# Performance work log

Measured on AMD Instinct MI355X. Metric: run time of the kernel, lower is better.

The kernel has to match this reference:

```python
import jax, jax.numpy as jnp
import numpy as np

EULER = 0.5772156649015329  # Euler-Mascheroni constant


def _expi_neg(t):
    """Ei(t) for t < 0, via Ei(t) = -E1(-t).

    E1 uses the power series for x < 8 and the asymptotic expansion for x >= 8.
    This replaces the scipy.special.expi CPU round-trip of the original module.
    """
    x = -t  # x > 0
    # --- series branch (x < 8): E1(x) = -gamma - ln(x) + sum_{k>=1} (-1)^{k+1} x^k/(k*k!)
    xs = jnp.minimum(x, 8.0)
    s = jnp.zeros_like(xs)
    term = xs  # (-1)^{k+1} xs^k / k!  starting at k=1
    for k in range(1, 31):
        s = s + term / k
        term = term * (-xs) / (k + 1)
    e1_small = -EULER - jnp.log(xs) + s
    # --- asymptotic branch (x >= 8): E1(x) ~ e^{-x}/x * sum_n (-1)^n n! / x^n
    xl = jnp.maximum(x, 8.0)
    a = jnp.ones_like(xl)
    acc = jnp.ones_like(xl)
    for n in range(1, 9):
        a = a * (-n) / xl
        acc = acc + a
    e1_large = jnp.exp(-xl) / xl * acc
    e1 = jnp.where(x < 8.0, e1_small, e1_large)
    return -e1


def _li(v):
    # logarithmic integral li(v) = Ei(ln v); constant w.r.t. params (scipy detaches in torch)
    return jax.lax.stop_gradient(_expi_neg(jnp.log(v)))


def _phi(u, var2, var3, var4, var5):
    log_term = jnp.log(1.0 - u)
    li_term = _li(1.0 - u)
    return (var2 / log_term
            + var3 * li_term
            + var4 * ((1.0 - u) / log_term - li_term)
            + var5 * ((1.0 - u) * (log_term + 1.0) / (2.0 * log_term ** 2) - li_term / 2.0))


def setup_inputs() -> dict:
    key = jax.random.key(0)
    B, L, D = 262144, 64, 32
    hidden = [128, 128, 64]
    ks = jax.random.split(key, 16)
    u = jax.random.uniform(ks[0], (B, L), dtype=jnp.float32, minval=1e-4, maxval=1.0 - 1e-4)
    dims = [L] + hidden + [D]
    inp = {"u": u}
    for i in range(4):
        inp[f"W{i}"] = jax.random.normal(ks[1 + 2 * i], (dims[i], dims[i + 1]), dtype=jnp.float32) / np.sqrt(dims[i]).astype(np.float32)
        inp[f"b{i}"] = jnp.zeros((dims[i + 1],), dtype=jnp.float32)
    for j in range(1, 7):
        inp[f"var{j}"] = jax.random.normal(ks[8 + j], (1, D), dtype=jnp.float32) * 0.1
    return inp


def reference(u, W0, b0, W1, b1, W2, b2, W3, b3, var1, var2, var3, var4, var5, var6):
    # MLP: three Linear+ReLU blocks then final Linear to dim_data
    h = u
    for W, b in ((W0, b0), (W1, b1), (W2, b2)):
        h = jax.nn.relu(h @ W + b)
    net = h @ W3 + b3  # (B, dim_data)
    D = net.shape[1]
    ud = u[:, :D]
    # spline corrections
    p01 = -4.0 * ud ** 5 + 5.0 * ud ** 4
    corr1 = jnp.nan_to_num(p01 * (var1 + _phi(ud, var2, var3, var4, var5)), nan=0.0)
    corr2 = var6 * (ud ** 3 - 2.0 * ud ** 2 + ud)
    net_tif = jax.nn.relu(net + corr1 + corr2)
    # inverse TIF activation: ((1 - u^2)/2)^{-x}
    return jnp.power((1.0 - ud ** 2) / 2.0, -net_tif)
```

## Files before the change

kernel.cpp:

```cpp
#include <hip/hip_runtime.h>
#include <hip/hip_bf16.h>
#include <math.h>

#define LN2_F 0.69314718055994531f
#define INV_LN2_F 1.44269504088896341f
#define REGION_HALFS 2048

typedef _Float16 half8 __attribute__((ext_vector_type(8)));
typedef _Float16 h4_t __attribute__((ext_vector_type(4)));
typedef __fp16 pk2_t __attribute__((ext_vector_type(2)));
typedef __attribute__((ext_vector_type(4))) float f32x4;
typedef __attribute__((ext_vector_type(8))) short short8;

#define MFMA16(a, b, c) __builtin_amdgcn_mfma_f32_16x16x32_f16((a), (b), (c), 0, 0, 0)

__global__ void prep_weights(const float* __restrict__ W0, const float* __restrict__ W1,
                             const float* __restrict__ W2, const float* __restrict__ W3,
                             short* __restrict__ ws) {
    int e = blockIdx.x * 256 + threadIdx.x;
    const float* W; int N, NT, base, ul;
    if (e < 1024)      { W = W0; N = 128; NT = 8; base = 0;     ul = e; }
    else if (e < 3072) { W = W1; N = 128; NT = 8; base = 8192;  ul = e - 1024; }
    else if (e < 4096) { W = W2; N = 64;  NT = 4; base = 24576; ul = e - 3072; }
    else if (e < 4352) { W = W3; N = 32;  NT = 2; base = 32768; ul = e - 4096; }
    else return;
    const int cp = ul >> 6, lane = ul & 63;
    const int s = cp / NT, ct = cp % NT;
    const int k0 = s * 32 + (lane >> 4) * 8;
    const int n = ct * 16 + (lane & 15);
    union { half8 h; short8 s; } v;
#pragma unroll
    for (int j = 0; j < 8; ++j) v.h[j] = (_Float16)W[(size_t)(k0 + j) * N + n];
    *(short8*)(ws + base + cp * 512 + lane * 8) = v.s;
}


__device__ __forceinline__ void lds_fence() {
    asm volatile("s_waitcnt lgkmcnt(0)" ::: "memory");
}

__device__ __forceinline__ half8 tr_read_ks(const _Float16* region, unsigned lane_off, int s) {
    h4_t lo, hi;
    asm volatile("ds_read_b64_tr_b16 %0, %2\n\t"
                 "ds_read_b64_tr_b16 %1, %2 offset:128"
                 : "=&v"(lo), "=&v"(hi)
                 : "v"((unsigned)(uintptr_t)region + lane_off + (unsigned)(s * 1024))
                 : "memory");
    return __builtin_shufflevector(lo, hi, 0, 1, 2, 3, 4, 5, 6, 7);
}

__device__ __forceinline__ void store_tile(_Float16* __restrict__ region, int ct_global,
                                           int m, int q, f32x4 v) {
    const int base = ct_global * 256 + (m >> 2) * 64 + (m & 3) * 16 + q * 4;
    pk2_t p0 = __builtin_amdgcn_cvt_pkrtz(v[0], v[1]);
    pk2_t p1 = __builtin_amdgcn_cvt_pkrtz(v[2], v[3]);
    h4_t h = {(_Float16)p0[0], (_Float16)p0[1], (_Float16)p1[0], (_Float16)p1[1]};
    h = __builtin_elementwise_max(h, (h4_t)(_Float16)0.0f);
    *(h4_t*)(region + base) = h;
}

template <int NK, int NT, int NC>
__device__ __forceinline__ void layer_half(const half8* __restrict__ wf,
                                           const float* __restrict__ bias, int ct0,
                                           const half8 (&af)[2][4], int lane, int m,
                                           f32x4 (&acc)[2][4]) {
#pragma unroll
    for (int c = 0; c < NC; ++c) {
        const float b = bias[(ct0 + c) * 16 + m];
        acc[0][c] = f32x4{b, b, b, b};
        acc[1][c] = f32x4{b, b, b, b};
    }
#pragma unroll
    for (int s = 0; s < NK; ++s) {
        half8 bf[4];
#pragma unroll
        for (int c = 0; c < NC; ++c) bf[c] = wf[(s * NT + ct0 + c) * 64 + lane];
#pragma unroll
        for (int c = 0; c < NC; ++c) {
            acc[0][c] = MFMA16(af[0][s], bf[c], acc[0][c]);
            acc[1][c] = MFMA16(af[1][s], bf[c], acc[1][c]);
        }
    }
}

__global__ __launch_bounds__(256, 5) void mlp_phi_mfma(
    const float* __restrict__ u,
    const float* __restrict__ b0, const float* __restrict__ b1,
    const float* __restrict__ b2, const float* __restrict__ b3,
    const short* __restrict__ ws,
    const float* __restrict__ var1, const float* __restrict__ var2,
    const float* __restrict__ var3, const float* __restrict__ var4,
    const float* __restrict__ var5, const float* __restrict__ var6,
    float* __restrict__ out) {
    __shared__ __align__(16) _Float16 lds[4 * 2 * REGION_HALFS];
    const int t = threadIdx.x, lane = t & 63, wave = t >> 6;
    const int m = lane & 15, q = lane >> 4;
    _Float16* lw = lds + wave * 2 * REGION_HALFS;
    const unsigned lane_rd = (unsigned)(q * 256 + m * 8);
    const size_t row0 = (size_t)blockIdx.x * 128 + wave * 32;

    const half8* wf0 = (const half8*)(ws);
    const half8* wf1 = (const half8*)(ws + 8192);
    const half8* wf2 = (const half8*)(ws + 24576);
    const half8* wf3 = (const half8*)(ws + 32768);

    half8 af[2][4];
    f32x4 acc[2][4];

#pragma unroll
    for (int mt = 0; mt < 2; ++mt) {
        const float* up = u + (row0 + mt * 16 + m) * 64;
#pragma unroll
        for (int s = 0; s < 2; ++s) {
            float4 v0a = *(const float4*)(up + s * 32 + q * 8);
            float4 v1a = *(const float4*)(up + s * 32 + q * 8 + 4);
            pk2_t p0 = __builtin_amdgcn_cvt_pkrtz(v0a.x, v0a.y);
            pk2_t p1 = __builtin_amdgcn_cvt_pkrtz(v0a.z, v0a.w);
            pk2_t p2 = __builtin_amdgcn_cvt_pkrtz(v1a.x, v1a.y);
            pk2_t p3 = __builtin_amdgcn_cvt_pkrtz(v1a.z, v1a.w);
            af[mt][s] = half8{(_Float16)p0[0], (_Float16)p0[1], (_Float16)p1[0], (_Float16)p1[1],
                              (_Float16)p2[0], (_Float16)p2[1], (_Float16)p3[0], (_Float16)p3[1]};
        }
    }

#pragma unroll
    for (int h = 0; h < 2; ++h) {
        layer_half<2, 8, 4>(wf0, b0, h * 4, af, lane, m, acc);
#pragma unroll
        for (int mt = 0; mt < 2; ++mt)
#pragma unroll
            for (int c = 0; c < 4; ++c)
                store_tile(lw + mt * REGION_HALFS, h * 4 + c, m, q, acc[mt][c]);
    }
    lds_fence();
#pragma unroll
    for (int mt = 0; mt < 2; ++mt)
#pragma unroll
        for (int s = 0; s < 4; ++s) af[mt][s] = tr_read_ks(lw + mt * REGION_HALFS, lane_rd, s);
    lds_fence();
    __builtin_amdgcn_sched_barrier(0);

#pragma unroll
    for (int h = 0; h < 2; ++h) {
        layer_half<4, 8, 4>(wf1, b1, h * 4, af, lane, m, acc);
#pragma unroll
        for (int mt = 0; mt < 2; ++mt)
#pragma unroll
            for (int c = 0; c < 4; ++c)
                store_tile(lw + mt * REGION_HALFS, h * 4 + c, m, q, acc[mt][c]);
    }
    lds_fence();
#pragma unroll
    for (int mt = 0; mt < 2; ++mt)
#pragma unroll
        for (int s = 0; s < 4; ++s) af[mt][s] = tr_read_ks(lw + mt * REGION_HALFS, lane_rd, s);
    lds_fence();
    __builtin_amdgcn_sched_barrier(0);

    layer_half<4, 4, 4>(wf2, b2, 0, af, lane, m, acc);
#pragma unroll
    for (int mt = 0; mt < 2; ++mt)
#pragma unroll
        for (int c = 0; c < 4; ++c)
            store_tile(lw + mt * REGION_HALFS, c, m, q, acc[mt][c]);
    lds_fence();
#pragma unroll
    for (int mt = 0; mt < 2; ++mt)
#pragma unroll
        for (int s = 0; s < 2; ++s) af[mt][s] = tr_read_ks(lw + mt * REGION_HALFS, lane_rd, s);
    lds_fence();
    __builtin_amdgcn_sched_barrier(0);

    layer_half<2, 2, 2>(wf3, b3, 0, af, lane, m, acc);

#pragma unroll
    for (int ot = 0; ot < 2; ++ot) {
        const int d = ot * 16 + m;
        const float v1 = var1[d], v6 = var6[d];
        const float v2p = var2[d] * INV_LN2_F;
        const float v4 = var4[d];
        const float v4p = v4 * INV_LN2_F;
        const float v5h = 0.5f * var5[d];
        const float v5hp = v5h * INV_LN2_F;
        const float c3 = var3[d] - v4 - v5h;
#pragma unroll
        for (int mt = 0; mt < 2; ++mt) {
            float ue[4];
#pragma unroll
            for (int r = 0; r < 4; ++r)
                ue[r] = u[(row0 + mt * 16 + q * 4 + r) * 64 + d];
#pragma unroll
            for (int r = 0; r < 4; ++r) {
                const size_t row = row0 + mt * 16 + q * 4 + r;
                const float net = acc[mt][ot][r];
                const float ud = ue[r];

                const float omu = 1.0f - ud;
                const float L = __log2f(omu);
                const float x = -L * LN2_F;
                const float RL = __builtin_amdgcn_rcpf(L);

                const float e1s = -__log2f(x) * LN2_F
                    + (-0.57721566f + x * (0.99999193f + x * (-0.24991055f
                    + x * (0.05519968f + x * (-0.00976004f + x * 0.00107857f)))));
                const float num = 0.2677737343f + x * (8.6347608925f + x * (18.0590169730f
                    + x * (8.5733287401f + x)));
                const float den = 3.9584969228f + x * (21.0996530827f + x * (25.6329561486f
                    + x * (9.5733223454f + x)));
                const float e1l = omu * num * __builtin_amdgcn_rcpf(x * den);
                const float li = -((x < 1.0f) ? e1s : e1l);

                const float phi = fmaf(v4p, omu, v2p) * RL
                                + (v5hp * omu * (L + INV_LN2_F)) * RL * RL
                                + c3 * li;

                const float ud2 = ud * ud;
                const float ud4 = ud2 * ud2;
                const float p01 = ud4 * fmaf(-4.0f, ud, 5.0f);
                const float corr1 = p01 * (v1 + phi);
                const float d1 = ud - 1.0f;
                const float corr2 = v6 * ud * d1 * d1;

                const float nt = fmaxf(net + corr1 + corr2, 0.0f);
                const float base = fmaf(-0.5f, ud2, 0.5f);
                out[row * 32 + d] = __builtin_amdgcn_exp2f(-nt * __log2f(base));
            }
        }
    }
}

extern "C" void kernel_launch(void* const* d_in, const int* in_sizes, int n_in,
                              void* d_out, int out_size, void* d_ws, size_t ws_size,
                              hipStream_t stream) {
    const float* u    = (const float*)d_in[0];
    const float* W0   = (const float*)d_in[1];
    const float* b0   = (const float*)d_in[2];
    const float* W1   = (const float*)d_in[3];
    const float* b1   = (const float*)d_in[4];
    const float* W2   = (const float*)d_in[5];
    const float* b2   = (const float*)d_in[6];
    const float* W3   = (const float*)d_in[7];
    const float* b3   = (const float*)d_in[8];
    const float* var1 = (const float*)d_in[9];
    const float* var2 = (const float*)d_in[10];
    const float* var3 = (const float*)d_in[11];
    const float* var4 = (const float*)d_in[12];
    const float* var5 = (const float*)d_in[13];
    const float* var6 = (const float*)d_in[14];
    float* out = (float*)d_out;
    short* ws = (short*)d_ws;

    prep_weights<<<dim3(17), dim3(256), 0, stream>>>(W0, W1, W2, W3, ws);

    const int B = in_sizes[0] / 64;
    const int blocks = B / 128;
    mlp_phi_mfma<<<dim3(blocks), dim3(256), 0, stream>>>(
        u, b0, b1, b2, b3, ws,
        var1, var2, var3, var4, var5, var6, out);
}
```

Measured before the change: 161.1 us.

## Give each wave 64 rows with 4 M-tiles, halving waves per block

Each wave now processes 64 rows (four 16-row M-tiles) and two output column tiles per pass, instead of 32 rows and four column tiles. The block shrinks to 128 threads with two waves, and launch bounds change to allow 3 blocks per CU. The aim is to reuse each loaded weight fragment across twice as many MFMAs, which cuts global and L2 weight traffic per row. The cost is more activation registers and per-wave LDS, and fewer resident waves, which may hurt latency hiding.

After: 158.3 us. Within noise of the previous version (-1.7%).

```diff
diff --git a/kernel.cpp b/kernel.cpp
--- a/kernel.cpp
+++ b/kernel.cpp
@@ -59,31 +59,31 @@
     *(h4_t*)(region + base) = h;
 }
 
-template <int NK, int NT, int NC>
-__device__ __forceinline__ void layer_half(const half8* __restrict__ wf,
-                                           const float* __restrict__ bias, int ct0,
-                                           const half8 (&af)[2][4], int lane, int m,
-                                           f32x4 (&acc)[2][4]) {
-#pragma unroll
-    for (int c = 0; c < NC; ++c) {
+template <int NK, int NT>
+__device__ __forceinline__ void layer_q(const half8* __restrict__ wf,
+                                        const float* __restrict__ bias, int ct0,
+                                        const half8 (&af)[4][4], int lane, int m,
+                                        f32x4 (&acc)[4][2]) {
+#pragma unroll
+    for (int c = 0; c < 2; ++c) {
         const float b = bias[(ct0 + c) * 16 + m];
-        acc[0][c] = f32x4{b, b, b, b};
-        acc[1][c] = f32x4{b, b, b, b};
+#pragma unroll
+        for (int mt = 0; mt < 4; ++mt) acc[mt][c] = f32x4{b, b, b, b};
     }
 #pragma unroll
     for (int s = 0; s < NK; ++s) {
-        half8 bf[4];
-#pragma unroll
-        for (int c = 0; c < NC; ++c) bf[c] = wf[(s * NT + ct0 + c) * 64 + lane];
-#pragma unroll
-        for (int c = 0; c < NC; ++c) {
-            acc[0][c] = MFMA16(af[0][s], bf[c], acc[0][c]);
-            acc[1][c] = MFMA16(af[1][s], bf[c], acc[1][c]);
-        }
-    }
-}
-
-__global__ __launch_bounds__(256, 5) void mlp_phi_mfma(
+        half8 bf[2];
+#pragma unroll
+        for (int c = 0; c < 2; ++c) bf[c] = wf[(s * NT + ct0 + c) * 64 + lane];
+#pragma unroll
+        for (int c = 0; c < 2; ++c)
+#pragma unroll
+            for (int mt = 0; mt < 4; ++mt)
+                acc[mt][c] = MFMA16(af[mt][s], bf[c], acc[mt][c]);
+    }
+}
+
+__global__ __launch_bounds__(128, 3) void mlp_phi_mfma(
     const float* __restrict__ u,
     const float* __restrict__ b0, const float* __restrict__ b1,
     const float* __restrict__ b2, const float* __restrict__ b3,
@@ -92,23 +92,23 @@
     const float* __restrict__ var3, const float* __restrict__ var4,
     const float* __restrict__ var5, const float* __restrict__ var6,
     float* __restrict__ out) {
-    __shared__ __align__(16) _Float16 lds[4 * 2 * REGION_HALFS];
+    __shared__ __align__(16) _Float16 lds[2 * 4 * REGION_HALFS];
     const int t = threadIdx.x, lane = t & 63, wave = t >> 6;
     const int m = lane & 15, q = lane >> 4;
-    _Float16* lw = lds + wave * 2 * REGION_HALFS;
+    _Float16* lw = lds + wave * 4 * REGION_HALFS;
     const unsigned lane_rd = (unsigned)(q * 256 + m * 8);
-    const size_t row0 = (size_t)blockIdx.x * 128 + wave * 32;
+    const size_t row0 = (size_t)blockIdx.x * 128 + wave * 64;
 
     const half8* wf0 = (const half8*)(ws);
     const half8* wf1 = (const half8*)(ws + 8192);
     const half8* wf2 = (const half8*)(ws + 24576);
     const half8* wf3 = (const half8*)(ws + 32768);
 
-    half8 af[2][4];
-    f32x4 acc[2][4];
-
-#pragma unroll
-    for (int mt = 0; mt < 2; ++mt) {
+    half8 af[4][4];
+    f32x4 acc[4][2];
+
+#pragma unroll
+    for (int mt = 0; mt < 4; ++mt) {
         const float* up = u + (row0 + mt * 16 + m) * 64;
 #pragma unroll
         for (int s = 0; s < 2; ++s) {
@@ -124,54 +124,57 @@
     }
 
 #pragma unroll
-    for (int h = 0; h < 2; ++h) {
-        layer_half<2, 8, 4>(wf0, b0, h * 4, af, lane, m, acc);
-#pragma unroll
-        for (int mt = 0; mt < 2; ++mt)
-#pragma unroll
-            for (int c = 0; c < 4; ++c)
-                store_tile(lw + mt * REGION_HALFS, h * 4 + c, m, q, acc[mt][c]);
-    }
-    lds_fence();
-#pragma unroll
-    for (int mt = 0; mt < 2; ++mt)
+    for (int qc = 0; qc < 4; ++qc) {
+        layer_q<2, 8>(wf0, b0, qc * 2, af, lane, m, acc);
+#pragma unroll
+        for (int mt = 0; mt < 4; ++mt)
+#pragma unroll
+            for (int c = 0; c < 2; ++c)
+                store_tile(lw + mt * REGION_HALFS, qc * 2 + c, m, q, acc[mt][c]);
+    }
+    lds_fence();
+#pragma unroll
+    for (int mt = 0; mt < 4; ++mt)
 #pragma unroll
         for (int s = 0; s < 4; ++s) af[mt][s] = tr_read_ks(lw + mt * REGION_HALFS, lane_rd, s);
     lds_fence();
     __builtin_amdgcn_sched_barrier(0);
 
 #pragma unroll
-    for (int h = 0; h < 2; ++h) {
-        layer_half<4, 8, 4>(wf1, b1, h * 4, af, lane, m, acc);
-#pragma unroll
-        for (int mt = 0; mt < 2; ++mt)
-#pragma unroll
-            for (int c = 0; c < 4; ++c)
-                store_tile(lw + mt * REGION_HALFS, h * 4 + c, m, q, acc[mt][c]);
-    }
-    lds_fence();
-#pragma unroll
-    for (int mt = 0; mt < 2; ++mt)
+    for (int qc = 0; qc < 4; ++qc) {
+        layer_q<4, 8>(wf1, b1, qc * 2, af, lane, m, acc);
+#pragma unroll
+        for (int mt = 0; mt < 4; ++mt)
+#pragma unroll
+            for (int c = 0; c < 2; ++c)
+                store_tile(lw + mt * REGION_HALFS, qc * 2 + c, m, q, acc[mt][c]);
+    }
+    lds_fence();
+#pragma unroll
+    for (int mt = 0; mt < 4; ++mt)
 #pragma unroll
         for (int s = 0; s < 4; ++s) af[mt][s] = tr_read_ks(lw + mt * REGION_HALFS, lane_rd, s);
     lds_fence();
     __builtin_amdgcn_sched_barrier(0);
 
-    layer_half<4, 4, 4>(wf2, b2, 0, af, lane, m, acc);
-#pragma unroll
-    for (int mt = 0; mt < 2; ++mt)
-#pragma unroll
-        for (int c = 0; c < 4; ++c)
-            store_tile(lw + mt * REGION_HALFS, c, m, q, acc[mt][c]);
-    lds_fence();
-#pragma unroll
-    for (int mt = 0; mt < 2; ++mt)
+#pragma unroll
+    for (int qc = 0; qc < 2; ++qc) {
+        layer_q<4, 4>(wf2, b2, qc * 2, af, lane, m, acc);
+#pragma unroll
+        for (int mt = 0; mt < 4; ++mt)
+#pragma unroll
+            for (int c = 0; c < 2; ++c)
+                store_tile(lw + mt * REGION_HALFS, qc * 2 + c, m, q, acc[mt][c]);
+    }
+    lds_fence();
+#pragma unroll
+    for (int mt = 0; mt < 4; ++mt)
 #pragma unroll
         for (int s = 0; s < 2; ++s) af[mt][s] = tr_read_ks(lw + mt * REGION_HALFS, lane_rd, s);
     lds_fence();
     __builtin_amdgcn_sched_barrier(0);
 
-    layer_half<2, 2, 2>(wf3, b3, 0, af, lane, m, acc);
+    layer_q<2, 2>(wf3, b3, 0, af, lane, m, acc);
 
 #pragma unroll
     for (int ot = 0; ot < 2; ++ot) {
@@ -184,7 +187,7 @@
         const float v5hp = v5h * INV_LN2_F;
         const float c3 = var3[d] - v4 - v5h;
 #pragma unroll
-        for (int mt = 0; mt < 2; ++mt) {
+        for (int mt = 0; mt < 4; ++mt) {
             float ue[4];
 #pragma unroll
             for (int r = 0; r < 4; ++r)
@@ -254,7 +257,7 @@
 
     const int B = in_sizes[0] / 64;
     const int blocks = B / 128;
-    mlp_phi_mfma<<<dim3(blocks), dim3(256), 0, stream>>>(
+    mlp_phi_mfma<<<dim3(blocks), dim3(128), 0, stream>>>(
         u, b0, b1, b2, b3, ws,
         var1, var2, var3, var4, var5, var6, out);
 }
```

## Stream weight fragments through per-wave LDS ring via async global_load_lds

Applied to the files above, without the earlier changes.

Weight fragments, which were loaded from global memory straight into registers, are now staged through a per-wave 3-slot LDS ring using global_load_lds, with vmcnt waits so later slices load while earlier ones run on MFMA. Bias and epilogue constants are hoisted into registers at kernel start. LDS use per block grows to 80 KB of dynamic shared memory and launch bounds drop from 5 to 2 blocks per CU. The aim is to hide weight-load latency, at the cost of lower occupancy and extra LDS traffic.

Result: no change. 163.4 us (+1.5%).

```diff
diff --git a/kernel.cpp b/kernel.cpp
--- a/kernel.cpp
+++ b/kernel.cpp
@@ -5,6 +5,9 @@
 #define LN2_F 0.69314718055994531f
 #define INV_LN2_F 1.44269504088896341f
 #define REGION_HALFS 2048
+#define SLOT_SH 2048
+#define WAVE_SH 10240
+#define BLOCK_LDS_B (4 * WAVE_SH * 2)
 
 typedef _Float16 half8 __attribute__((ext_vector_type(8)));
 typedef _Float16 h4_t __attribute__((ext_vector_type(4)));
@@ -59,31 +62,76 @@
     *(h4_t*)(region + base) = h;
 }
 
+__device__ __forceinline__ void gll_frag(const short* g, short* l) {
+    __builtin_amdgcn_global_load_lds(
+        (const __attribute__((address_space(1))) void*)g,
+        (__attribute__((address_space(3))) void*)l, 16, 0, 0);
+}
+
+template <int N>
+__device__ __forceinline__ void wait_vmcnt() {
+    asm volatile("s_waitcnt vmcnt(%0)" :: "n"(N) : "memory");
+}
+
 template <int NK, int NT, int NC>
-__device__ __forceinline__ void layer_half(const half8* __restrict__ wf,
-                                           const float* __restrict__ bias, int ct0,
-                                           const half8 (&af)[2][4], int lane, int m,
-                                           f32x4 (&acc)[2][4]) {
+__device__ __forceinline__ void layer_ring(const short* __restrict__ wl, int ct0,
+                                           short* __restrict__ ring, int lane8,
+                                           const float* bias,
+                                           const half8 (&af)[2][4], f32x4 (&acc)[2][4]) {
+    static_assert(NK == 2 || NK == 4, "");
+    __builtin_amdgcn_sched_barrier(0);
+#define ISSUE(S, SLOT)                                                            \
+    do {                                                                          \
+        _Pragma("unroll") for (int c = 0; c < NC; ++c)                            \
+            gll_frag(wl + (((S) * NT + ct0 + c) << 9) + lane8,                    \
+                     ring + (SLOT) * SLOT_SH + (c << 9));                         \
+    } while (0)
+#define DO_SLICE(S, SLOT)                                                         \
+    do {                                                                          \
+        half8 bf[NC];                                                             \
+        _Pragma("unroll") for (int c = 0; c < NC; ++c)                            \
+            bf[c] = *(const half8*)(ring + (SLOT) * SLOT_SH + (c << 9) + lane8);  \
+        _Pragma("unroll") for (int c = 0; c < NC; ++c) {                          \
+            acc[0][c] = MFMA16(af[0][S], bf[c], acc[0][c]);                       \
+            acc[1][c] = MFMA16(af[1][S], bf[c], acc[1][c]);                       \
+        }                                                                         \
+    } while (0)
+
 #pragma unroll
     for (int c = 0; c < NC; ++c) {
-        const float b = bias[(ct0 + c) * 16 + m];
+        const float b = bias[c];
         acc[0][c] = f32x4{b, b, b, b};
         acc[1][c] = f32x4{b, b, b, b};
     }
-#pragma unroll
-    for (int s = 0; s < NK; ++s) {
-        half8 bf[4];
-#pragma unroll
-        for (int c = 0; c < NC; ++c) bf[c] = wf[(s * NT + ct0 + c) * 64 + lane];
-#pragma unroll
-        for (int c = 0; c < NC; ++c) {
-            acc[0][c] = MFMA16(af[0][s], bf[c], acc[0][c]);
-            acc[1][c] = MFMA16(af[1][s], bf[c], acc[1][c]);
-        }
-    }
-}
-
-__global__ __launch_bounds__(256, 5) void mlp_phi_mfma(
+    ISSUE(0, 0);
+    ISSUE(1, 1);
+    if constexpr (NK == 4) ISSUE(2, 2);
+
+    wait_vmcnt<(NK == 4 ? 2 * NC : NC)>();
+    __builtin_amdgcn_sched_barrier(0);
+    DO_SLICE(0, 0);
+    if constexpr (NK == 2) {
+        wait_vmcnt<0>();
+        __builtin_amdgcn_sched_barrier(0);
+        DO_SLICE(1, 1);
+    } else {
+        __builtin_amdgcn_sched_barrier(0);
+        ISSUE(3, 0);
+        wait_vmcnt<2 * NC>();
+        __builtin_amdgcn_sched_barrier(0);
+        DO_SLICE(1, 1);
+        wait_vmcnt<NC>();
+        __builtin_amdgcn_sched_barrier(0);
+        DO_SLICE(2, 2);
+        wait_vmcnt<0>();
+        __builtin_amdgcn_sched_barrier(0);
+        DO_SLICE(3, 0);
+    }
+#undef ISSUE
+#undef DO_SLICE
+}
+
+__global__ __launch_bounds__(256, 2) void mlp_phi_mfma(
     const float* __restrict__ u,
     const float* __restrict__ b0, const float* __restrict__ b1,
     const float* __restrict__ b2, const float* __restrict__ b3,
@@ -92,20 +140,44 @@
     const float* __restrict__ var3, const float* __restrict__ var4,
     const float* __restrict__ var5, const float* __restrict__ var6,
     float* __restrict__ out) {
-    __shared__ __align__(16) _Float16 lds[4 * 2 * REGION_HALFS];
+    extern __shared__ __align__(16) short smem[];
     const int t = threadIdx.x, lane = t & 63, wave = t >> 6;
     const int m = lane & 15, q = lane >> 4;
-    _Float16* lw = lds + wave * 2 * REGION_HALFS;
+    const int lane8 = lane * 8;
+    short* wbase = smem + wave * WAVE_SH;
+    _Float16* act = (_Float16*)wbase;
+    short* ring = wbase + 4096;
     const unsigned lane_rd = (unsigned)(q * 256 + m * 8);
     const size_t row0 = (size_t)blockIdx.x * 128 + wave * 32;
 
-    const half8* wf0 = (const half8*)(ws);
-    const half8* wf1 = (const half8*)(ws + 8192);
-    const half8* wf2 = (const half8*)(ws + 24576);
-    const half8* wf3 = (const half8*)(ws + 32768);
+    const short* wl0 = ws;
+    const short* wl1 = ws + 8192;
+    const short* wl2 = ws + 24576;
+    const short* wl3 = ws + 32768;
 
     half8 af[2][4];
     f32x4 acc[2][4];
+
+    float bb0v[8], bb1v[8], bb2v[4], bb3v[2];
+#pragma unroll
+    for (int ct = 0; ct < 8; ++ct) bb0v[ct] = b0[ct * 16 + m];
+#pragma unroll
+    for (int ct = 0; ct < 8; ++ct) bb1v[ct] = b1[ct * 16 + m];
+#pragma unroll
+    for (int ct = 0; ct < 4; ++ct) bb2v[ct] = b2[ct * 16 + m];
+#pragma unroll
+    for (int ct = 0; ct < 2; ++ct) bb3v[ct] = b3[ct * 16 + m];
+
+    float ev1[2], ev2p[2], ev4[2], ev4p[2], ev5h[2], ev5hp[2], ev6[2], ec3[2];
+#pragma unroll
+    for (int ot = 0; ot < 2; ++ot) {
+        const int d = ot * 16 + m;
+        ev1[ot] = var1[d]; ev6[ot] = var6[d];
+        ev2p[ot] = var2[d] * INV_LN2_F;
+        ev4[ot] = var4[d]; ev4p[ot] = ev4[ot] * INV_LN2_F;
+        ev5h[ot] = 0.5f * var5[d]; ev5hp[ot] = ev5h[ot] * INV_LN2_F;
+        ec3[ot] = var3[d] - ev4[ot] - ev5h[ot];
+    }
 
 #pragma unroll
     for (int mt = 0; mt < 2; ++mt) {
@@ -123,66 +195,63 @@
         }
     }
 
-#pragma unroll
-    for (int h = 0; h < 2; ++h) {
-        layer_half<2, 8, 4>(wf0, b0, h * 4, af, lane, m, acc);
-#pragma unroll
-        for (int mt = 0; mt < 2; ++mt)
-#pragma unroll
-            for (int c = 0; c < 4; ++c)
-                store_tile(lw + mt * REGION_HALFS, h * 4 + c, m, q, acc[mt][c]);
-    }
-    lds_fence();
-#pragma unroll
-    for (int mt = 0; mt < 2; ++mt)
-#pragma unroll
-        for (int s = 0; s < 4; ++s) af[mt][s] = tr_read_ks(lw + mt * REGION_HALFS, lane_rd, s);
-    lds_fence();
-    __builtin_amdgcn_sched_barrier(0);
-
-#pragma unroll
-    for (int h = 0; h < 2; ++h) {
-        layer_half<4, 8, 4>(wf1, b1, h * 4, af, lane, m, acc);
-#pragma unroll
-        for (int mt = 0; mt < 2; ++mt)
-#pragma unroll
-            for (int c = 0; c < 4; ++c)
-                store_tile(lw + mt * REGION_HALFS, h * 4 + c, m, q, acc[mt][c]);
-    }
-    lds_fence();
-#pragma unroll
-    for (int mt = 0; mt < 2; ++mt)
-#pragma unroll
-        for (int s = 0; s < 4; ++s) af[mt][s] = tr_read_ks(lw + mt * REGION_HALFS, lane_rd, s);
-    lds_fence();
-    __builtin_amdgcn_sched_barrier(0);
-
-    layer_half<4, 4, 4>(wf2, b2, 0, af, lane, m, acc);
-#pragma unroll
-    for (int mt = 0; mt < 2; ++mt)
-#pragma unroll
-        for (int c = 0; c < 4; ++c)
-            store_tile(lw + mt * REGION_HALFS, c, m, q, acc[mt][c]);
-    lds_fence();
-#pragma unroll
-    for (int mt = 0; mt < 2; ++mt)
-#pragma unroll
-        for (int s = 0; s < 2; ++s) af[mt][s] = tr_read_ks(lw + mt * REGION_HALFS, lane_rd, s);
-    lds_fence();
-    __builtin_amdgcn_sched_barrier(0);
-
-    layer_half<2, 2, 2>(wf3, b3, 0, af, lane, m, acc);
+    layer_ring<2, 8, 4>(wl0, 0, ring, lane8, bb0v + 0, af, acc);
+#pragma unroll
+    for (int mt = 0; mt < 2; ++mt)
+#pragma unroll
+        for (int c = 0; c < 4; ++c) store_tile(act + mt * REGION_HALFS, c, m, q, acc[mt][c]);
+    layer_ring<2, 8, 4>(wl0, 4, ring, lane8, bb0v + 4, af, acc);
+#pragma unroll
+    for (int mt = 0; mt < 2; ++mt)
+#pragma unroll
+        for (int c = 0; c < 4; ++c) store_tile(act + mt * REGION_HALFS, 4 + c, m, q, acc[mt][c]);
+    lds_fence();
+#pragma unroll
+    for (int mt = 0; mt < 2; ++mt)
+#pragma unroll
+        for (int s = 0; s < 4; ++s) af[mt][s] = tr_read_ks(act + mt * REGION_HALFS, lane_rd, s);
+    lds_fence();
+    __builtin_amdgcn_sched_barrier(0);
+
+    layer_ring<4, 8, 4>(wl1, 0, ring, lane8, bb1v + 0, af, acc);
+#pragma unroll
+    for (int mt = 0; mt < 2; ++mt)
+#pragma unroll
+        for (int c = 0; c < 4; ++c) store_tile(act + mt * REGION_HALFS, c, m, q, acc[mt][c]);
+    layer_ring<4, 8, 4>(wl1, 4, ring, lane8, bb1v + 4, af, acc);
+#pragma unroll
+    for (int mt = 0; mt < 2; ++mt)
+#pragma unroll
+        for (int c = 0; c < 4; ++c) store_tile(act + mt * REGION_HALFS, 4 + c, m, q, acc[mt][c]);
+    lds_fence();
+#pragma unroll
+    for (int mt = 0; mt < 2; ++mt)
+#pragma unroll
+        for (int s = 0; s < 4; ++s) af[mt][s] = tr_read_ks(act + mt * REGION_HALFS, lane_rd, s);
+    lds_fence();
+    __builtin_amdgcn_sched_barrier(0);
+
+    layer_ring<4, 4, 4>(wl2, 0, ring, lane8, bb2v, af, acc);
+#pragma unroll
+    for (int mt = 0; mt < 2; ++mt)
+#pragma unroll
+        for (int c = 0; c < 4; ++c) store_tile(act + mt * REGION_HALFS, c, m, q, acc[mt][c]);
+    lds_fence();
+#pragma unroll
+    for (int mt = 0; mt < 2; ++mt)
+#pragma unroll
+        for (int s = 0; s < 2; ++s) af[mt][s] = tr_read_ks(act + mt * REGION_HALFS, lane_rd, s);
+    lds_fence();
+    __builtin_amdgcn_sched_barrier(0);
+
+    layer_ring<2, 2, 2>(wl3, 0, ring, lane8, bb3v, af, acc);
 
 #pragma unroll
     for (int ot = 0; ot < 2; ++ot) {
         const int d = ot * 16 + m;
-        const float v1 = var1[d], v6 = var6[d];
-        const float v2p = var2[d] * INV_LN2_F;
-        const float v4 = var4[d];
-        const float v4p = v4 * INV_LN2_F;
-        const float v5h = 0.5f * var5[d];
-        const float v5hp = v5h * INV_LN2_F;
-        const float c3 = var3[d] - v4 - v5h;
+        const float v1 = ev1[ot], v6 = ev6[ot];
+        const float v2p = ev2p[ot], v4p = ev4p[ot], v5hp = ev5hp[ot];
+        const float c3 = ec3[ot];
 #pragma unroll
         for (int mt = 0; mt < 2; ++mt) {
             float ue[4];
@@ -252,9 +321,12 @@
 
     prep_weights<<<dim3(17), dim3(256), 0, stream>>>(W0, W1, W2, W3, ws);
 
+    hipFuncSetAttribute(reinterpret_cast<const void*>(mlp_phi_mfma),
+                        hipFuncAttributeMaxDynamicSharedMemorySize, BLOCK_LDS_B);
+
     const int B = in_sizes[0] / 64;
     const int blocks = B / 128;
-    mlp_phi_mfma<<<dim3(blocks), dim3(256), 0, stream>>>(
+    mlp_phi_mfma<<<dim3(blocks), dim3(256), BLOCK_LDS_B, stream>>>(
         u, b0, b1, b2, b3, ws,
         var1, var2, var3, var4, var5, var6, out);
 }
```
